# Kernel optimization log

Hardware: AMD Instinct MI355X
Metric: run time of the kernel (lower is better)

## Reference

```python
import jax, jax.numpy as jnp
import numpy as np

SEQ = 8          # sequence_size
C = 128          # in_channels / factor (hidden + input channels)
BN_EPS = 1e-5


def setup_inputs() -> dict:
    key = jax.random.key(0)
    k1, k2 = jax.random.split(key)
    x = jax.random.normal(k1, (32, C, 64, 64), dtype=jnp.float32)          # (B*T, C, H, W)
    w_conv = jax.random.normal(k2, (4 * C, 2 * C, 3, 3), dtype=jnp.float32) * 0.05  # OIHW
    b_conv = jnp.zeros((4 * C,), dtype=jnp.float32)
    gamma = jnp.ones((C,), dtype=jnp.float32)
    beta = jnp.zeros((C,), dtype=jnp.float32)
    run_mean = jnp.zeros((C,), dtype=jnp.float32)
    run_var = jnp.ones((C,), dtype=jnp.float32)
    return {"x": x, "w_conv": w_conv, "b_conv": b_conv, "gamma": gamma,
            "beta": beta, "run_mean": run_mean, "run_var": run_var}


def _convlstm_scan(x_seq, w_conv, b_conv):
    # x_seq: (B, T, C, H, W); zero initial (h, c) states (reset path)
    B, T, Cc, H, W = x_seq.shape
    h0 = jnp.zeros((B, Cc, H, W), x_seq.dtype)
    c0 = jnp.zeros((B, Cc, H, W), x_seq.dtype)

    def step(carry, x_t):
        h, c = carry
        z = jax.lax.conv_general_dilated(
            jnp.concatenate([x_t, h], axis=1), w_conv,
            window_strides=(1, 1), padding='SAME',
            dimension_numbers=('NCHW', 'OIHW', 'NCHW'))
        z = z + b_conv[None, :, None, None]
        i, f, o, g = jnp.split(z, 4, axis=1)
        c_next = jax.nn.sigmoid(f) * c + jax.nn.sigmoid(i) * jnp.tanh(g)
        h_next = jax.nn.sigmoid(o) * jnp.tanh(c_next)
        return (h_next, c_next), h_next

    _, hs = jax.lax.scan(step, (h0, c0), jnp.swapaxes(x_seq, 0, 1))  # hs: (T, B, C, H, W)
    return jnp.swapaxes(hs, 0, 1)  # (B, T, C, H, W)


def reference(x, w_conv, b_conv, gamma, beta, run_mean, run_var):
    BT, Cc, H, W = x.shape
    x_seq = x.reshape(BT // SEQ, SEQ, Cc, H, W)
    hs = _convlstm_scan(x_seq, w_conv, b_conv)           # (B, T, C, H, W)
    out = hs.reshape(-1, Cc, H, W)                        # (B*T, C, H, W)
    # BatchNorm2d (eval mode: running stats) + ReLU
    inv = jax.lax.rsqrt(run_var + BN_EPS)
    out = (out - run_mean[None, :, None, None]) * (inv * gamma)[None, :, None, None] \
          + beta[None, :, None, None]
    return jax.nn.relu(out)
```

## Files before the change

### kernel.cpp

```cpp
#include <hip/hip_runtime.h>
#include <hip/hip_bf16.h>
#include <math.h>

typedef __attribute__((ext_vector_type(8))) short bf16x8;
typedef __attribute__((ext_vector_type(4))) float f32x4;

#define FRAME_PAD (66*66*128)

#define GLOAD_LDS16(g, l) \
    __builtin_amdgcn_global_load_lds((const __attribute__((address_space(1))) void*)(g), \
                                     (__attribute__((address_space(3))) void*)(l), 16, 0, 0)

#define WAITV6    asm volatile("s_waitcnt vmcnt(6)" ::: "memory")
#define WAITV0    asm volatile("s_waitcnt vmcnt(0)" ::: "memory")
#define WAITLGKM0 asm volatile("s_waitcnt lgkmcnt(0)" ::: "memory")
#define SBAR      __builtin_amdgcn_s_barrier()

__device__ __forceinline__ float sigmoidf_(float x) { return 1.0f / (1.0f + __expf(-x)); }
__device__ __forceinline__ float tanhf_(float x) {
    x = fminf(fmaxf(x, -15.0f), 15.0f);
    float e = __expf(2.0f * x);
    return (e - 1.0f) / (e + 1.0f);
}

__global__ void wt_kernel(const float* __restrict__ w, __hip_bfloat16* __restrict__ wt)
{
    int idx = blockIdx.x * 256 + threadIdx.x;
    if (idx >= 9 * 512 * 256) return;
    int ic  = idx & 255;
    int n   = (idx >> 8) & 511;
    int tap = idx >> 17;
    int c = n >> 2, g = n & 3;
    int oc = g * 128 + c;
    wt[idx] = __float2bfloat16(w[((size_t)oc * 256 + (size_t)ic) * 9 + tap]);
}

__global__ void xpose_kernel(const float* __restrict__ x, __hip_bfloat16* __restrict__ x_pad)
{
    __shared__ float tile[128][65];
    const int f = blockIdx.x >> 6;
    const int y = blockIdx.x & 63;
    const int tid = threadIdx.x;
    const float* src = x + (size_t)f * 524288 + (size_t)y * 64;
    #pragma unroll
    for (int it = 0; it < 32; ++it) {
        int c  = it * 4 + (tid >> 6);
        int xc = tid & 63;
        tile[c][xc] = src[(size_t)c * 4096 + xc];
    }
    __syncthreads();
    __hip_bfloat16* dst = x_pad + (size_t)f * FRAME_PAD + (size_t)((y + 1) * 66 + 1) * 128;
    #pragma unroll
    for (int it = 0; it < 16; ++it) {
        int xr = it * 4 + (tid >> 6);
        int c2 = (tid & 63) * 2;
        __hip_bfloat162 v;
        v.x = __float2bfloat16(tile[c2][xr]);
        v.y = __float2bfloat16(tile[c2 + 1][xr]);
        *(__hip_bfloat162*)(dst + (size_t)xr * 128 + c2) = v;
    }
}

__global__ __launch_bounds__(512, 2)
void conv_gemm(const __hip_bfloat16* __restrict__ x_pad,
               const __hip_bfloat16* __restrict__ h_pad,
               const __hip_bfloat16* __restrict__ wt,
               const float* __restrict__ bias,
               float* __restrict__ c_state, int t)
{
    __shared__ alignas(16) __hip_bfloat16 S_s[2][256 * 64];
    __shared__ alignas(16) __hip_bfloat16 W_s[2][128 * 64];
    const int tid  = threadIdx.x;
    const int wv   = tid >> 6;
    const int lane = tid & 63;

    const int F    = blockIdx.x;
    const int tile = (F >> 3) + (F & 7) * 32;
    const int n0   = (tile & 3) * 128;
    const int mblk = tile >> 2;
    const int b    = mblk >> 4;
    const int y0   = (mblk & 15) * 4;
    const int m0   = mblk * 256;

    const __hip_bfloat16* xf = x_pad + (size_t)(b * 8 + t) * FRAME_PAD;
    const __hip_bfloat16* hf = h_pad + (size_t)(b * 9 + t) * FRAME_PAD;

    int aOff[4], bOff[2];
    #pragma unroll
    for (int j = 0; j < 4; ++j) {
        int sid = j * 512 + tid;
        int row = sid >> 3;
        int q   = (sid & 7) ^ (row & 7);
        aOff[j] = ((y0 + (row >> 6)) * 66 + (row & 63)) * 128 + q * 8;
    }
    #pragma unroll
    for (int j = 0; j < 2; ++j) {
        int sid = j * 512 + tid;
        int row = sid >> 3;
        int q   = (sid & 7) ^ (row & 7);
        bOff[j] = (n0 + row) * 256 + q * 8;
    }

    auto STAGE = [&](__hip_bfloat16* Sl, __hip_bfloat16* Wl, int kt) {
        const int tap = kt >> 2;
        const int icq = (kt & 3) * 64;
        const int dy = tap / 3, dx = tap % 3;
        const __hip_bfloat16* asrc =
            (icq < 128 ? xf + icq : hf + (icq - 128)) + (dy * 66 + dx) * 128;
        #pragma unroll
        for (int j = 0; j < 4; ++j)
            GLOAD_LDS16(asrc + aOff[j], Sl + (size_t)(j * 512 + tid) * 8);
        const __hip_bfloat16* bsrc = wt + tap * 131072 + icq;
        #pragma unroll
        for (int j = 0; j < 2; ++j)
            GLOAD_LDS16(bsrc + bOff[j], Wl + (size_t)(j * 512 + tid) * 8);
    };

    const int wm = wv >> 1, wn = wv & 1;
    const int fr = lane & 15, fq = lane >> 4;
    const int slot = (fq ^ (fr & 7)) * 8;
    const int sOff0 = (wm * 64 + fr) * 64 + slot, sOff1 = sOff0 ^ 32;
    const int wOff0 = (wn * 64 + fr) * 64 + slot, wOff1 = wOff0 ^ 32;

    f32x4 acc[4][4] = {};

    auto ITER = [&](__hip_bfloat16* Sb, __hip_bfloat16* Wb, int kt) {
        if (kt < 35) { WAITV6; } else { WAITV0; }
        SBAR;
        bf16x8 w0[4], w1[4], s0[4], s1[4];
        #pragma unroll
        for (int ri = 0; ri < 4; ++ri) {
            w0[ri] = *(const bf16x8*)(Wb + wOff0 + ri * 1024);
            w1[ri] = *(const bf16x8*)(Wb + wOff1 + ri * 1024);
        }
        #pragma unroll
        for (int ci = 0; ci < 4; ++ci) {
            s0[ci] = *(const bf16x8*)(Sb + sOff0 + ci * 1024);
            s1[ci] = *(const bf16x8*)(Sb + sOff1 + ci * 1024);
        }
        __builtin_amdgcn_s_setprio(1);
        #pragma unroll
        for (int ri = 0; ri < 4; ++ri)
            #pragma unroll
            for (int ci = 0; ci < 4; ++ci)
                acc[ri][ci] = __builtin_amdgcn_mfma_f32_16x16x32_bf16(w0[ri], s0[ci], acc[ri][ci], 0, 0, 0);
        __builtin_amdgcn_s_setprio(0);
        WAITLGKM0;
        __builtin_amdgcn_sched_barrier(0);
        SBAR;
        if (kt < 34) STAGE(Sb, Wb, kt + 2);
        __builtin_amdgcn_s_setprio(1);
        #pragma unroll
        for (int ri = 0; ri < 4; ++ri)
            #pragma unroll
            for (int ci = 0; ci < 4; ++ci)
                acc[ri][ci] = __builtin_amdgcn_mfma_f32_16x16x32_bf16(w1[ri], s1[ci], acc[ri][ci], 0, 0, 0);
        __builtin_amdgcn_s_setprio(0);
    };

    STAGE(S_s[0], W_s[0], 0);
    STAGE(S_s[1], W_s[1], 1);
    #pragma unroll 1
    for (int kt = 0; kt < 36; kt += 2) {
        ITER(S_s[0], W_s[0], kt);
        ITER(S_s[1], W_s[1], kt + 1);
    }

    const int c0    = (n0 >> 2) + wn * 16;
    const int mcol0 = m0 + wm * 64 + fr;
    __hip_bfloat16* hout = (__hip_bfloat16*)h_pad + (size_t)(b * 9 + t + 1) * FRAME_PAD;
    #pragma unroll
    for (int ri = 0; ri < 4; ++ri) {
        const int c = c0 + ri * 4 + fq;
        const float bi  = bias[c];
        const float bfv = bias[128 + c];
        const float bo  = bias[256 + c];
        const float bg  = bias[384 + c];
        float* csrow = c_state + (size_t)c * 16384;
        #pragma unroll
        for (int ci = 0; ci < 4; ++ci) {
            const int m = mcol0 + ci * 16;
            const int s = m & 4095;
            const float cold = csrow[m];
            const float zi = acc[ri][ci][0] + bi;
            const float zf = acc[ri][ci][1] + bfv;
            const float zo = acc[ri][ci][2] + bo;
            const float zg = acc[ri][ci][3] + bg;
            const float cn = sigmoidf_(zf) * cold + sigmoidf_(zi) * tanhf_(zg);
            const float h  = sigmoidf_(zo) * tanhf_(cn);
            csrow[m] = cn;
            hout[(size_t)(((s >> 6) + 1) * 66 + (s & 63) + 1) * 128 + c] = __float2bfloat16(h);
        }
    }
}

__global__ void bn_out_kernel(const __hip_bfloat16* __restrict__ h_pad,
                              const float* __restrict__ gamma, const float* __restrict__ beta,
                              const float* __restrict__ rmean, const float* __restrict__ rvar,
                              float* __restrict__ out)
{
    __shared__ float tile[64][130];
    __shared__ float sc_s[128], sh_s[128];
    const int fo  = blockIdx.x >> 6;
    const int y   = blockIdx.x & 63;
    const int tid = threadIdx.x;
    if (tid < 128) {
        float sc = gamma[tid] * rsqrtf(rvar[tid] + 1e-5f);
        sc_s[tid] = sc;
        sh_s[tid] = beta[tid] - rmean[tid] * sc;
    }
    const int b = fo >> 3, t = fo & 7;
    const __hip_bfloat16* src =
        h_pad + (size_t)(b * 9 + 1 + t) * FRAME_PAD + (size_t)((y + 1) * 66 + 1) * 128;
    #pragma unroll
    for (int it = 0; it < 32; ++it) {
        int xr = it * 2 + (tid >> 7);
        int c  = tid & 127;
        tile[xr][c] = __bfloat162float(src[(size_t)xr * 128 + c]);
    }
    __syncthreads();
    float* dst = out + (size_t)fo * 524288 + (size_t)y * 64;
    #pragma unroll
    for (int it = 0; it < 32; ++it) {
        int c  = it * 4 + (tid >> 6);
        int xc = tid & 63;
        float v = tile[xc][c] * sc_s[c] + sh_s[c];
        dst[(size_t)c * 4096 + xc] = fmaxf(v, 0.0f);
    }
}

extern "C" void kernel_launch(void* const* d_in, const int* in_sizes, int n_in,
                              void* d_out, int out_size, void* d_ws, size_t ws_size,
                              hipStream_t stream)
{
    const float* x      = (const float*)d_in[0];
    const float* w_conv = (const float*)d_in[1];
    const float* b_conv = (const float*)d_in[2];
    const float* gamma  = (const float*)d_in[3];
    const float* beta   = (const float*)d_in[4];
    const float* rmean  = (const float*)d_in[5];
    const float* rvar   = (const float*)d_in[6];
    float* out = (float*)d_out;

    if (ws_size < 86577152u) return;

    char* ws = (char*)d_ws;
    __hip_bfloat16* Wt    = (__hip_bfloat16*)(ws);
    __hip_bfloat16* x_pad = (__hip_bfloat16*)(ws + 2359296);
    __hip_bfloat16* h_pad = (__hip_bfloat16*)(ws + 38043648);
    float* c_state        = (float*)(ws + 78188544);

    hipMemsetAsync(x_pad, 0, 35684352, stream);
    hipMemsetAsync(h_pad, 0, 40144896, stream);
    hipMemsetAsync(c_state, 0, 8388608, stream);

    wt_kernel<<<4608, 256, 0, stream>>>(w_conv, Wt);
    xpose_kernel<<<2048, 256, 0, stream>>>(x, x_pad);

    for (int t = 0; t < 8; ++t) {
        conv_gemm<<<256, 512, 0, stream>>>(x_pad, h_pad, Wt, b_conv, c_state, t);
    }
    bn_out_kernel<<<2048, 256, 0, stream>>>(h_pad, gamma, beta, rmean, rvar, out);
}
```

Baseline: 403.4 us.

## Skip zero-h half at t=0, triple-buffer A tiles, vectorize transposes, zero borders only

The first timestep gets its own conv_gemm instantiation that runs only the input-channel half of the K loop and treats the old cell state as zero, since h and c start at zero. The GEMM main loop now uses a three-stage rotating A buffer with loads split across the two MFMA halves. Full-buffer memsets are replaced by a small kernel that zeroes only the padding borders, with h_pad relaid out without the zero frame. The xpose and bn_out kernels switch to float4 and bf16x8 vector accesses, and bn_out applies BN and ReLU before its transpose. The extra LDS buffer and extra barriers may lower occupancy or add synchronization cost.

```diff
diff --git a/kernel.cpp b/kernel.cpp
--- a/kernel.cpp
+++ b/kernel.cpp
@@ -21,6 +21,14 @@
     x = fminf(fmaxf(x, -15.0f), 15.0f);
     float e = __expf(2.0f * x);
     return (e - 1.0f) / (e + 1.0f);
+}
+__device__ __forceinline__ float b2f_(short u) {
+    unsigned int v = ((unsigned int)(unsigned short)u) << 16;
+    return __builtin_bit_cast(float, v);
+}
+__device__ __forceinline__ short f2b_(float f) {
+    __hip_bfloat16 hb = __float2bfloat16(f);
+    return *reinterpret_cast<short*>(&hb);
 }
 
 __global__ void wt_kernel(const float* __restrict__ w, __hip_bfloat16* __restrict__ wt)
@@ -35,32 +43,57 @@
     wt[idx] = __float2bfloat16(w[((size_t)oc * 256 + (size_t)ic) * 9 + tap]);
 }
 
+__global__ void border_kernel(__hip_bfloat16* __restrict__ x_pad,
+                              __hip_bfloat16* __restrict__ h_pad)
+{
+    const int fr = blockIdx.x;
+    __hip_bfloat16* base = (fr < 32) ? x_pad + (size_t)fr * FRAME_PAD
+                                     : h_pad + (size_t)(fr - 32) * FRAME_PAD;
+    bf16x8 z = {};
+    for (int u = threadIdx.x; u < 2112; u += 256) {
+        int half = (u >= 1056) ? 1 : 0;
+        int v = u - half * 1056;
+        *(bf16x8*)(base + (size_t)(half * 65 * 66) * 128 + (size_t)v * 8) = z;
+    }
+    for (int u = threadIdx.x; u < 2048; u += 256) {
+        int yy = 1 + (u >> 5);
+        int r = u & 31;
+        int side = r >> 4, c16 = r & 15;
+        *(bf16x8*)(base + (size_t)(yy * 66 + side * 65) * 128 + (size_t)c16 * 8) = z;
+    }
+}
+
 __global__ void xpose_kernel(const float* __restrict__ x, __hip_bfloat16* __restrict__ x_pad)
 {
-    __shared__ float tile[128][65];
+    __shared__ float tile[64][129];
     const int f = blockIdx.x >> 6;
     const int y = blockIdx.x & 63;
     const int tid = threadIdx.x;
     const float* src = x + (size_t)f * 524288 + (size_t)y * 64;
     #pragma unroll
-    for (int it = 0; it < 32; ++it) {
-        int c  = it * 4 + (tid >> 6);
-        int xc = tid & 63;
-        tile[c][xc] = src[(size_t)c * 4096 + xc];
+    for (int it = 0; it < 8; ++it) {
+        int c  = it * 16 + (tid >> 4);
+        int xq = tid & 15;
+        float4 v = *(const float4*)(src + (size_t)c * 4096 + xq * 4);
+        tile[xq * 4 + 0][c] = v.x;
+        tile[xq * 4 + 1][c] = v.y;
+        tile[xq * 4 + 2][c] = v.z;
+        tile[xq * 4 + 3][c] = v.w;
     }
     __syncthreads();
     __hip_bfloat16* dst = x_pad + (size_t)f * FRAME_PAD + (size_t)((y + 1) * 66 + 1) * 128;
-    #pragma unroll
-    for (int it = 0; it < 16; ++it) {
-        int xr = it * 4 + (tid >> 6);
-        int c2 = (tid & 63) * 2;
-        __hip_bfloat162 v;
-        v.x = __float2bfloat16(tile[c2][xr]);
-        v.y = __float2bfloat16(tile[c2 + 1][xr]);
-        *(__hip_bfloat162*)(dst + (size_t)xr * 128 + c2) = v;
-    }
-}
-
+    const int g = tid & 15;
+    #pragma unroll
+    for (int it = 0; it < 4; ++it) {
+        int xr = it * 16 + (tid >> 4);
+        bf16x8 o;
+        #pragma unroll
+        for (int e = 0; e < 8; ++e) o[e] = f2b_(tile[xr][g * 8 + e]);
+        *(bf16x8*)(dst + (size_t)xr * 128 + g * 8) = o;
+    }
+}
+
+template<bool T0>
 __global__ __launch_bounds__(512, 2)
 void conv_gemm(const __hip_bfloat16* __restrict__ x_pad,
                const __hip_bfloat16* __restrict__ h_pad,
@@ -68,11 +101,12 @@
                const float* __restrict__ bias,
                float* __restrict__ c_state, int t)
 {
-    __shared__ alignas(16) __hip_bfloat16 S_s[2][256 * 64];
+    __shared__ alignas(16) __hip_bfloat16 S_s[3][256 * 64];
     __shared__ alignas(16) __hip_bfloat16 W_s[2][128 * 64];
     const int tid  = threadIdx.x;
     const int wv   = tid >> 6;
     const int lane = tid & 63;
+    const int KT   = T0 ? 18 : 36;
 
     const int F    = blockIdx.x;
     const int tile = (F >> 3) + (F & 7) * 32;
@@ -83,7 +117,7 @@
     const int m0   = mblk * 256;
 
     const __hip_bfloat16* xf = x_pad + (size_t)(b * 8 + t) * FRAME_PAD;
-    const __hip_bfloat16* hf = h_pad + (size_t)(b * 9 + t) * FRAME_PAD;
+    const __hip_bfloat16* hf = h_pad + (size_t)(b * 8 + (T0 ? 0 : t - 1)) * FRAME_PAD;
 
     int aOff[4], bOff[2];
     #pragma unroll
@@ -101,15 +135,21 @@
         bOff[j] = (n0 + row) * 256 + q * 8;
     }
 
-    auto STAGE = [&](__hip_bfloat16* Sl, __hip_bfloat16* Wl, int kt) {
-        const int tap = kt >> 2;
-        const int icq = (kt & 3) * 64;
+    auto stageA = [&](__hip_bfloat16* Sl, int kt, int j0, int j1) {
+        int tap, icq;
+        const __hip_bfloat16* sb;
+        if constexpr (T0) { tap = kt >> 1; icq = (kt & 1) * 64; sb = xf + icq; }
+        else { tap = kt >> 2; icq = (kt & 3) * 64;
+               sb = (icq < 128) ? (xf + icq) : (hf + (icq - 128)); }
         const int dy = tap / 3, dx = tap % 3;
-        const __hip_bfloat16* asrc =
-            (icq < 128 ? xf + icq : hf + (icq - 128)) + (dy * 66 + dx) * 128;
-        #pragma unroll
-        for (int j = 0; j < 4; ++j)
-            GLOAD_LDS16(asrc + aOff[j], Sl + (size_t)(j * 512 + tid) * 8);
+        const __hip_bfloat16* a = sb + (dy * 66 + dx) * 128;
+        for (int j = j0; j < j1; ++j)
+            GLOAD_LDS16(a + aOff[j], Sl + (size_t)(j * 512 + tid) * 8);
+    };
+    auto stageW = [&](__hip_bfloat16* Wl, int kt) {
+        int tap, icq;
+        if constexpr (T0) { tap = kt >> 1; icq = (kt & 1) * 64; }
+        else { tap = kt >> 2; icq = (kt & 3) * 64; }
         const __hip_bfloat16* bsrc = wt + tap * 131072 + icq;
         #pragma unroll
         for (int j = 0; j < 2; ++j)
@@ -124,20 +164,26 @@
 
     f32x4 acc[4][4] = {};
 
-    auto ITER = [&](__hip_bfloat16* Sb, __hip_bfloat16* Wb, int kt) {
-        if (kt < 35) { WAITV6; } else { WAITV0; }
+    __hip_bfloat16 *Sr = &S_s[0][0], *Sn = &S_s[1][0], *Sf = &S_s[2][0];
+    __hip_bfloat16 *Wr = &W_s[0][0], *Wn = &W_s[1][0];
+
+    stageA(Sr, 0, 0, 4); stageW(Wr, 0);
+    stageA(Sn, 1, 0, 4); stageW(Wn, 1);
+    WAITV6;
+    SBAR;
+
+    #pragma unroll 1
+    for (int kt = 0; kt < KT; ++kt) {
+        bf16x8 w0[4], w1[4], s0[4], s1[4];
+        #pragma unroll
+        for (int ri = 0; ri < 4; ++ri) w0[ri] = *(const bf16x8*)(Wr + wOff0 + ri * 1024);
+        #pragma unroll
+        for (int ci = 0; ci < 4; ++ci) s0[ci] = *(const bf16x8*)(Sr + sOff0 + ci * 1024);
+        #pragma unroll
+        for (int ri = 0; ri < 4; ++ri) w1[ri] = *(const bf16x8*)(Wr + wOff1 + ri * 1024);
+        if (kt < KT - 2) stageA(Sf, kt + 2, 0, 2);
         SBAR;
-        bf16x8 w0[4], w1[4], s0[4], s1[4];
-        #pragma unroll
-        for (int ri = 0; ri < 4; ++ri) {
-            w0[ri] = *(const bf16x8*)(Wb + wOff0 + ri * 1024);
-            w1[ri] = *(const bf16x8*)(Wb + wOff1 + ri * 1024);
-        }
-        #pragma unroll
-        for (int ci = 0; ci < 4; ++ci) {
-            s0[ci] = *(const bf16x8*)(Sb + sOff0 + ci * 1024);
-            s1[ci] = *(const bf16x8*)(Sb + sOff1 + ci * 1024);
-        }
+        WAITLGKM0;
         __builtin_amdgcn_s_setprio(1);
         #pragma unroll
         for (int ri = 0; ri < 4; ++ri)
@@ -145,10 +191,12 @@
             for (int ci = 0; ci < 4; ++ci)
                 acc[ri][ci] = __builtin_amdgcn_mfma_f32_16x16x32_bf16(w0[ri], s0[ci], acc[ri][ci], 0, 0, 0);
         __builtin_amdgcn_s_setprio(0);
+        SBAR;
+        #pragma unroll
+        for (int ci = 0; ci < 4; ++ci) s1[ci] = *(const bf16x8*)(Sr + sOff1 + ci * 1024);
+        if (kt < KT - 2) { stageA(Sf, kt + 2, 2, 4); stageW(Wr, kt + 2); }
+        SBAR;
         WAITLGKM0;
-        __builtin_amdgcn_sched_barrier(0);
-        SBAR;
-        if (kt < 34) STAGE(Sb, Wb, kt + 2);
         __builtin_amdgcn_s_setprio(1);
         #pragma unroll
         for (int ri = 0; ri < 4; ++ri)
@@ -156,19 +204,15 @@
             for (int ci = 0; ci < 4; ++ci)
                 acc[ri][ci] = __builtin_amdgcn_mfma_f32_16x16x32_bf16(w1[ri], s1[ci], acc[ri][ci], 0, 0, 0);
         __builtin_amdgcn_s_setprio(0);
-    };
-
-    STAGE(S_s[0], W_s[0], 0);
-    STAGE(S_s[1], W_s[1], 1);
-    #pragma unroll 1
-    for (int kt = 0; kt < 36; kt += 2) {
-        ITER(S_s[0], W_s[0], kt);
-        ITER(S_s[1], W_s[1], kt + 1);
+        if (kt < KT - 2) { WAITV6; } else { WAITV0; }
+        SBAR;
+        __hip_bfloat16* tp = Sr; Sr = Sn; Sn = Sf; Sf = tp;
+        __hip_bfloat16* tw = Wr; Wr = Wn; Wn = tw;
     }
 
     const int c0    = (n0 >> 2) + wn * 16;
     const int mcol0 = m0 + wm * 64 + fr;
-    __hip_bfloat16* hout = (__hip_bfloat16*)h_pad + (size_t)(b * 9 + t + 1) * FRAME_PAD;
+    __hip_bfloat16* hout = (__hip_bfloat16*)h_pad + (size_t)(b * 8 + t) * FRAME_PAD;
     #pragma unroll
     for (int ri = 0; ri < 4; ++ri) {
         const int c = c0 + ri * 4 + fq;
@@ -181,7 +225,7 @@
         for (int ci = 0; ci < 4; ++ci) {
             const int m = mcol0 + ci * 16;
             const int s = m & 4095;
-            const float cold = csrow[m];
+            const float cold = T0 ? 0.0f : csrow[m];
             const float zi = acc[ri][ci][0] + bi;
             const float zf = acc[ri][ci][1] + bfv;
             const float zo = acc[ri][ci][2] + bo;
@@ -199,7 +243,7 @@
                               const float* __restrict__ rmean, const float* __restrict__ rvar,
                               float* __restrict__ out)
 {
-    __shared__ float tile[64][130];
+    __shared__ float tile[64][129];
     __shared__ float sc_s[128], sh_s[128];
     const int fo  = blockIdx.x >> 6;
     const int y   = blockIdx.x & 63;
@@ -209,23 +253,33 @@
         sc_s[tid] = sc;
         sh_s[tid] = beta[tid] - rmean[tid] * sc;
     }
-    const int b = fo >> 3, t = fo & 7;
+    __syncthreads();
     const __hip_bfloat16* src =
-        h_pad + (size_t)(b * 9 + 1 + t) * FRAME_PAD + (size_t)((y + 1) * 66 + 1) * 128;
-    #pragma unroll
-    for (int it = 0; it < 32; ++it) {
-        int xr = it * 2 + (tid >> 7);
-        int c  = tid & 127;
-        tile[xr][c] = __bfloat162float(src[(size_t)xr * 128 + c]);
+        h_pad + (size_t)fo * FRAME_PAD + (size_t)((y + 1) * 66 + 1) * 128;
+    const int g = tid & 15;
+    float sc[8], sh[8];
+    #pragma unroll
+    for (int e = 0; e < 8; ++e) { sc[e] = sc_s[g * 8 + e]; sh[e] = sh_s[g * 8 + e]; }
+    #pragma unroll
+    for (int it = 0; it < 4; ++it) {
+        int xr = it * 16 + (tid >> 4);
+        bf16x8 v = *(const bf16x8*)(src + (size_t)xr * 128 + g * 8);
+        #pragma unroll
+        for (int e = 0; e < 8; ++e)
+            tile[xr][g * 8 + e] = fmaxf(b2f_(v[e]) * sc[e] + sh[e], 0.0f);
     }
     __syncthreads();
     float* dst = out + (size_t)fo * 524288 + (size_t)y * 64;
     #pragma unroll
-    for (int it = 0; it < 32; ++it) {
-        int c  = it * 4 + (tid >> 6);
-        int xc = tid & 63;
-        float v = tile[xc][c] * sc_s[c] + sh_s[c];
-        dst[(size_t)c * 4096 + xc] = fmaxf(v, 0.0f);
+    for (int it = 0; it < 8; ++it) {
+        int c  = it * 16 + (tid >> 4);
+        int xq = tid & 15;
+        float4 o;
+        o.x = tile[xq * 4 + 0][c];
+        o.y = tile[xq * 4 + 1][c];
+        o.z = tile[xq * 4 + 2][c];
+        o.w = tile[xq * 4 + 3][c];
+        *(float4*)(dst + (size_t)c * 4096 + xq * 4) = o;
     }
 }
 
@@ -242,23 +296,21 @@
     const float* rvar   = (const float*)d_in[6];
     float* out = (float*)d_out;
 
-    if (ws_size < 86577152u) return;
+    if (ws_size < 82116608u) return;
 
     char* ws = (char*)d_ws;
     __hip_bfloat16* Wt    = (__hip_bfloat16*)(ws);
     __hip_bfloat16* x_pad = (__hip_bfloat16*)(ws + 2359296);
     __hip_bfloat16* h_pad = (__hip_bfloat16*)(ws + 38043648);
-    float* c_state        = (float*)(ws + 78188544);
-
-    hipMemsetAsync(x_pad, 0, 35684352, stream);
-    hipMemsetAsync(h_pad, 0, 40144896, stream);
-    hipMemsetAsync(c_state, 0, 8388608, stream);
+    float* c_state        = (float*)(ws + 73728000);
 
     wt_kernel<<<4608, 256, 0, stream>>>(w_conv, Wt);
     xpose_kernel<<<2048, 256, 0, stream>>>(x, x_pad);
-
-    for (int t = 0; t < 8; ++t) {
-        conv_gemm<<<256, 512, 0, stream>>>(x_pad, h_pad, Wt, b_conv, c_state, t);
-    }
+    border_kernel<<<64, 256, 0, stream>>>(x_pad, h_pad);
+
+    conv_gemm<true><<<256, 512, 0, stream>>>(x_pad, h_pad, Wt, b_conv, c_state, 0);
+    for (int t = 1; t < 8; ++t)
+        conv_gemm<false><<<256, 512, 0, stream>>>(x_pad, h_pad, Wt, b_conv, c_state, t);
+
     bn_out_kernel<<<2048, 256, 0, stream>>>(h_pad, gamma, beta, rmean, rvar, out);
 }
```

Result: faster. 382.1 us (-5.3%).
